# Performance work log

Measured on AMD Instinct MI355X. Metric: run time of the kernel, lower is better.

Reference implementation:

```python
import jax, jax.numpy as jnp
from jax import lax
import numpy as np

MAL = 10  # max_atom_len

def _conv1d(x, w, b):
    # x: [N,C,L], w: [O,I,K], 'same' padding for K=3 (pad 1)
    pad = (w.shape[-1] - 1) // 2
    y = lax.conv_general_dilated(x, w, (1,), [(pad, pad)], dimension_numbers=('NCH', 'OIH', 'NCH'))
    return y + b[None, :, None]

def _maxpool2(x):
    return lax.reduce_window(x, -jnp.inf, lax.max, (1, 1, 2), (1, 1, 2), 'VALID')

def setup_inputs():
    key = jax.random.key(0)
    ks = jax.random.split(key, 32)
    def p(i, shape):
        return 0.05 * jax.random.normal(ks[i], shape, jnp.float32)
    bs, seq, C, L = 128, 128, 6, 20
    D, H = 64, 256
    return {
        'x': jax.random.normal(ks[0], (bs, seq, C, L), jnp.float32),
        'imu_mask': jnp.ones((bs, seq, C, L), jnp.float32),
        'imu_len': jax.random.randint(ks[1], (bs,), 1, seq + 1),
        'c1_w': p(2, (16, 6, 3)), 'c1_b': p(3, (16,)),
        'c2_w': p(4, (32, 16, 3)), 'c2_b': p(5, (32,)),
        'c3_w': p(6, (32, 32, 3)), 'c3_b': p(7, (32,)),
        'br_w': p(8, (64, D)), 'br_b': p(9, (D,)),
        'f1_w': p(10, (D, H)), 'f1_b': p(11, (H,)),
        'f2_w': p(12, (H, D)), 'f2_b': p(13, (D,)),
        'd1_w': p(14, (16, 32, 5)), 'd1_b': p(15, (32,)),
        'd2_w': p(16, (6, 32, 3)), 'd2_b': p(17, (6,)),
        'ae1_w': p(18, (32, D, 3)), 'ae1_b': p(19, (32,)),
        'ae2_w': p(20, (16, 32, 3)), 'ae2_b': p(21, (16,)),
        'ae3_w': p(22, (80, 32)), 'ae3_b': p(23, (32,)),
        'ad1_w': p(24, (32, H)), 'ad1_b': p(25, (H,)),
        'ad2_w': p(26, (H, 6 * MAL * seq)), 'ad2_b': p(27, (6 * MAL * seq,)),
    }

def reference(x, imu_mask, c1_w, c1_b, c2_w, c2_b, c3_w, c3_b, br_w, br_b,
              f1_w, f1_b, f2_w, f2_b, d1_w, d1_b, d2_w, d2_b,
              ae1_w, ae1_b, ae2_w, ae2_b, ae3_w, ae3_b,
              ad1_w, ad1_b, ad2_w, ad2_b, imu_len):
    bs, seq, C, L = x.shape
    N = bs * seq
    # --- CNN encoder: [N,6,20] -> [N,32,2] -> flat 64 ---
    h = _maxpool2(jax.nn.relu(_conv1d(x.reshape(N, C, L), c1_w, c1_b)))  # [N,16,10]
    h = _maxpool2(jax.nn.relu(_conv1d(h, c2_w, c2_b)))                   # [N,32,5]
    h = _maxpool2(jax.nn.relu(_conv1d(h, c3_w, c3_b)))                   # [N,32,2]
    cnn_out = h.reshape(N, -1)
    bridge_out = jax.nn.sigmoid(cnn_out @ br_w + br_b)  # [N,D]
    D = bridge_out.shape[1]
    # --- forecast branch ---
    forcast_in3 = bridge_out.reshape(bs, seq, D)
    shft = jnp.pad(forcast_in3, ((0, 0), (1, 0), (0, 0)))[:, :-1]  # shift right by 1
    fmask = jnp.ones((bs, seq, D), jnp.float32).at[:, 0, :].set(0.0).reshape(N, D)
    fmask = fmask * imu_mask[:, :, 0, 0].reshape(N, 1)
    forcast_in = forcast_in3.reshape(N, D)
    feat = jax.nn.relu(shft.reshape(N, D) @ f1_w + f1_b)
    forcast = feat @ f2_w + f2_b
    forcast_loss = jnp.mean(jnp.square((forcast - forcast_in) * fmask), axis=1)  # [N]
    loss2d = forcast_loss.reshape(bs, seq)
    # --- host-side segmentation (mirrors original sort/argwhere/.item() loop) ---
    scores = np.asarray(forcast_loss * fmask[:, 0])
    k = int(scores.shape[0] * 0.2)
    cutoff = float(np.sort(scores)[::-1][:k].min())
    l2 = np.asarray(loss2d)
    seg_lists = []
    for b in range(bs):
        idxs = np.nonzero(l2[b] > cutoff)[0]
        segs = []
        if idxs.shape[0] > 0:
            for i in range(idxs.shape[0] - 1):
                if int(idxs[i + 1] - idxs[i]) > MAL:
                    cur = int(idxs[i]); segs.append(cur)
                    while cur < int(idxs[i + 1]):
                        cur += MAL
                        if cur >= int(idxs[i + 1]):
                            break
                        segs.append(cur)
                else:
                    segs.append(int(idxs[i]))
            segs.append(int(idxs[-1]))
        seg_lists.append(segs)
    # --- build variable-length atoms (left-pad / left-crop to fixed widths) ---
    bridge_np = np.asarray(forcast_in3)
    x_np = np.asarray(x)
    Wtot = MAL * seq
    feats, atoms, masks = [], [], []
    for b in range(bs):
        last = 0
        for e in seg_lists[b]:
            f = bridge_np[b, last:e]  # [n,D]
            pad = MAL - f.shape[0]
            fp = np.concatenate([np.zeros((pad, D), np.float32), f], 0) if pad >= 0 else f[-pad:]
            a = x_np[b, last:e].transpose(1, 0, 2).reshape(C, -1)  # [C, n*L]
            ap = Wtot - a.shape[1]
            if ap >= 0:
                apad = np.concatenate([np.zeros((C, ap), np.float32), a], 1)
                m = np.zeros((C, Wtot), np.float32); m[:, ap:] = 1.0
            else:
                apad = a[:, -ap:]; m = np.ones((C, Wtot), np.float32)
            feats.append(fp); atoms.append(apad); masks.append(m)
            last = e
    if len(feats) == 0:  # degenerate guard
        feats = [np.zeros((MAL, D), np.float32)]
        atoms = [np.zeros((C, Wtot), np.float32)]
        masks = [np.zeros((C, Wtot), np.float32)]
    A = len(feats)
    atom_features = jnp.asarray(np.stack(feats)).swapaxes(1, 2)  # [A,D,MAL]
    imu_atoms = jnp.asarray(np.stack(atoms))                      # [A,C,Wtot]
    imu_atoms_mask = jnp.asarray(np.stack(masks))
    # --- atom encoder / decoder ---
    ha = _maxpool2(jax.nn.relu(_conv1d(atom_features, ae1_w, ae1_b)))  # [A,32,5]
    ha = jax.nn.relu(_conv1d(ha, ae2_w, ae2_b))                        # [A,16,5]
    emb = ha.reshape(A, -1) @ ae3_w + ae3_b                            # [A,32]
    hd = jax.nn.relu(emb @ ad1_w + ad1_b)
    atom_gen = (hd @ ad2_w + ad2_b).reshape(A, C, Wtot)
    # --- imu decoder: [N,16,4] -> [N,6,20] ---
    bridge_resh = bridge_out.reshape(N, 16, 4)
    # non-overlapping transpose conv (kernel=stride=5): 4 -> 20
    g = jnp.einsum('nci,cok->noik', bridge_resh, d1_w).reshape(N, 32, 20)
    g = jax.nn.relu(g + d1_b[None, :, None])
    imu_gen = _conv1d(g, d2_w, d2_b).reshape(bs, seq, C, L)
    return (imu_gen, atom_gen, imu_atoms_mask, imu_atoms, bridge_resh,
            forcast_in, forcast, fmask, forcast_loss)
```

## Files before the change

### kernel.cpp

```cpp
#include <hip/hip_runtime.h>
#include <math.h>


#define NWIN 16384
#define SEQ  128
#define BS   128
#define KSEL 3276
#define SEGSTRIDE 160
#define RECCAP 18432

typedef __attribute__((ext_vector_type(8))) short short8v;
typedef __attribute__((ext_vector_type(4))) float float4v;

__device__ inline unsigned short bf16rne(float f) {
    unsigned u = __float_as_uint(f);
    unsigned r = u + 0x7FFFu + ((u >> 16) & 1u);
    return (unsigned short)(r >> 16);
}

__global__ __launch_bounds__(256) void k_encoder(
        const float* __restrict__ x,
        const float* __restrict__ c1w, const float* __restrict__ c1b,
        const float* __restrict__ c2w, const float* __restrict__ c2b,
        const float* __restrict__ c3w, const float* __restrict__ c3b,
        const float* __restrict__ brw, const float* __restrict__ brb,
        float* __restrict__ bridge, float* __restrict__ out_resh,
        float* __restrict__ out_fin) {
    __shared__ float c1wt[288];
    __shared__ float c2wt[1536];
    __shared__ float c3wt[3072];
    __shared__ float brws[4096];
    __shared__ float c1bs[16], c2bs[32], c3bs[32], brbs[64];
    __shared__ float xs[4][128], c1s[4][160], c2s[4][160], c3s[4][64];

    int tid = threadIdx.x;
    for (int i = tid; i < 288; i += 256) {
        int oc = i / 18, r = i - oc * 18, ic = r / 3, dk = r - ic * 3;
        c1wt[(ic * 3 + dk) * 16 + oc] = c1w[i];
    }
    for (int i = tid; i < 1536; i += 256) {
        int oc = i / 48, r = i - oc * 48, ic = r / 3, dk = r - ic * 3;
        c2wt[(ic * 3 + dk) * 32 + oc] = c2w[i];
    }
    for (int i = tid; i < 3072; i += 256) {
        int oc = i / 96, r = i - oc * 96, ic = r / 3, dk = r - ic * 3;
        c3wt[(ic * 3 + dk) * 32 + oc] = c3w[i];
    }
    for (int i = tid; i < 4096; i += 256) brws[i] = brw[i];
    if (tid < 16) c1bs[tid] = c1b[tid];
    else if (tid < 48) c2bs[tid - 16] = c2b[tid - 16];
    else if (tid < 80) c3bs[tid - 48] = c3b[tid - 48];
    else if (tid < 144) brbs[tid - 80] = brb[tid - 80];

    int wv = tid >> 6, lane = tid & 63;
    int n = blockIdx.x * 4 + wv;
    const float* xr = x + (size_t)n * 120;
    if (lane < 60) ((float2*)&xs[wv][0])[lane] = ((const float2*)xr)[lane];
    __syncthreads();

    {
        int oc = lane >> 2, tg = lane & 3;
        float bb = c1bs[oc];
        float acc[3][2];
#pragma unroll
        for (int j = 0; j < 3; ++j) { acc[j][0] = bb; acc[j][1] = bb; }
        for (int ic = 0; ic < 6; ++ic) {
            float w0 = c1wt[(ic * 3 + 0) * 16 + oc];
            float w1 = c1wt[(ic * 3 + 1) * 16 + oc];
            float w2 = c1wt[(ic * 3 + 2) * 16 + oc];
            const float* ar = &xs[wv][ic * 20];
#pragma unroll
            for (int j = 0; j < 3; ++j) {
                int t = tg + 4 * j;
                if (t < 10) {
#pragma unroll
                    for (int q = 0; q < 2; ++q) {
                        int p = 2 * t + q;
                        float a0 = (p >= 1) ? ar[p - 1] : 0.f;
                        float a1 = ar[p];
                        float a2 = (p + 1 < 20) ? ar[p + 1] : 0.f;
                        acc[j][q] += a0 * w0 + a1 * w1 + a2 * w2;
                    }
                }
            }
        }
#pragma unroll
        for (int j = 0; j < 3; ++j) {
            int t = tg + 4 * j;
            if (t < 10) c1s[wv][oc * 10 + t] = fmaxf(fmaxf(acc[j][0], acc[j][1]), 0.f);
        }
    }
    __syncthreads();

    {
        int oc = lane >> 1, tg = lane & 1;
        float bb = c2bs[oc];
        float acc[3][2];
#pragma unroll
        for (int j = 0; j < 3; ++j) { acc[j][0] = bb; acc[j][1] = bb; }
        for (int ic = 0; ic < 16; ++ic) {
            float w0 = c2wt[(ic * 3 + 0) * 32 + oc];
            float w1 = c2wt[(ic * 3 + 1) * 32 + oc];
            float w2 = c2wt[(ic * 3 + 2) * 32 + oc];
            const float* ar = &c1s[wv][ic * 10];
#pragma unroll
            for (int j = 0; j < 3; ++j) {
                int t = tg + 2 * j;
                if (t < 5) {
#pragma unroll
                    for (int q = 0; q < 2; ++q) {
                        int p = 2 * t + q;
                        float a0 = (p >= 1) ? ar[p - 1] : 0.f;
                        float a1 = ar[p];
                        float a2 = (p + 1 < 10) ? ar[p + 1] : 0.f;
                        acc[j][q] += a0 * w0 + a1 * w1 + a2 * w2;
                    }
                }
            }
        }
#pragma unroll
        for (int j = 0; j < 3; ++j) {
            int t = tg + 2 * j;
            if (t < 5) c2s[wv][oc * 5 + t] = fmaxf(fmaxf(acc[j][0], acc[j][1]), 0.f);
        }
    }
    __syncthreads();

    {
        int oc = lane >> 1, tp = lane & 1;
        float bb = c3bs[oc];
        float acc0 = bb, acc1 = bb;
        for (int ic = 0; ic < 32; ++ic) {
            float w0 = c3wt[(ic * 3 + 0) * 32 + oc];
            float w1 = c3wt[(ic * 3 + 1) * 32 + oc];
            float w2 = c3wt[(ic * 3 + 2) * 32 + oc];
            const float* ar = &c2s[wv][ic * 5];
            {
                int p = 2 * tp;
                float a0 = (p >= 1) ? ar[p - 1] : 0.f;
                acc0 += a0 * w0 + ar[p] * w1 + ar[p + 1] * w2;
            }
            {
                int p = 2 * tp + 1;
                acc1 += ar[p - 1] * w0 + ar[p] * w1 + ((p + 1 < 5) ? ar[p + 1] : 0.f) * w2;
            }
        }
        c3s[wv][lane] = fmaxf(fmaxf(acc0, acc1), 0.f);
    }
    __syncthreads();

    {
        float acc = brbs[lane];
        for (int i = 0; i < 64; ++i) acc += c3s[wv][i] * brws[i * 64 + lane];
        float v = 1.f / (1.f + expf(-acc));
        size_t o = (size_t)n * 64 + lane;
        bridge[o] = v; out_resh[o] = v; out_fin[o] = v;
    }
}

__global__ void k_f1(const float* __restrict__ bridge, const float* __restrict__ w,
                     const float* __restrict__ b, float* __restrict__ feat) {
    int n = blockIdx.x, h = threadIdx.x;
    int s = n & (SEQ - 1);
    float acc = b[h];
    if (s > 0) {
        const float* br = bridge + (n - 1) * 64;
        for (int d = 0; d < 64; ++d) acc += br[d] * w[d * 256 + h];
    }
    feat[n * 256 + h] = fmaxf(acc, 0.f);
}

__global__ void k_f2_loss(const float* __restrict__ feat, const float* __restrict__ bridge,
                          const float* __restrict__ w, const float* __restrict__ b,
                          const float* __restrict__ imu_mask,
                          float* __restrict__ out_fc, float* __restrict__ out_fmask,
                          float* __restrict__ out_loss, float* __restrict__ scores) {
    int n = blockIdx.x, d = threadIdx.x;
    const float* fr = feat + n * 256;
    float acc = b[d];
    for (int h = 0; h < 256; ++h) acc += fr[h] * w[h * 64 + d];
    out_fc[n * 64 + d] = acc;
    int s = n & (SEQ - 1);
    float mval = (s == 0) ? 0.f : imu_mask[(size_t)n * 120];
    out_fmask[n * 64 + d] = mval;
    float diff = (acc - bridge[n * 64 + d]) * mval;
    float sq = diff * diff;
#pragma unroll
    for (int off = 32; off; off >>= 1) sq += __shfl_down(sq, off);
    if (d == 0) {
        float loss = sq * (1.f / 64.f);
        out_loss[n] = loss;
        scores[n] = loss * mval;
    }
}

__global__ void k_select(const float* __restrict__ scores, float* __restrict__ cutoff) {
    __shared__ unsigned hist[256];
    __shared__ unsigned sh_prefix;
    __shared__ int sh_k;
    int tid = threadIdx.x;
    if (tid == 0) { sh_prefix = 0u; sh_k = KSEL; }
    __syncthreads();
    for (int shift = 24; shift >= 0; shift -= 8) {
        hist[tid] = 0u;
        __syncthreads();
        unsigned prefix = sh_prefix;
        unsigned pmask = (shift == 24) ? 0u : (0xFFFFFFFFu << (shift + 8));
        for (int i = tid; i < NWIN; i += 256) {
            unsigned u = __float_as_uint(scores[i]);
            if ((u & pmask) == prefix) atomicAdd(&hist[(u >> shift) & 255u], 1u);
        }
        __syncthreads();
        if (tid == 0) {
            int kk = sh_k;
            for (int bin = 255; bin >= 0; --bin) {
                int c = (int)hist[bin];
                if (kk <= c) { sh_prefix = prefix | ((unsigned)bin << shift); sh_k = kk; break; }
                kk -= c;
            }
        }
        __syncthreads();
    }
    if (tid == 0) *cutoff = __uint_as_float(sh_prefix);
}

__global__ void k_segments(const float* __restrict__ loss, const float* __restrict__ cutoff_p,
                           int* __restrict__ segs, int* __restrict__ counts) {
    int b = threadIdx.x;
    if (b >= BS) return;
    float cutoff = *cutoff_p;
    int* my = segs + b * SEGSTRIDE;
    int cnt = 0, prev = 0;
    bool has = false;
    for (int s = 0; s < SEQ; ++s) {
        if (loss[b * SEQ + s] > cutoff) {
            if (has) {
                if (s - prev > 10) {
                    my[cnt++] = prev;
                    int cur = prev;
                    while (cur < s) {
                        cur += 10;
                        if (cur >= s) break;
                        my[cnt++] = cur;
                    }
                } else {
                    my[cnt++] = prev;
                }
            }
            has = true; prev = s;
        }
    }
    if (has) my[cnt++] = prev;
    counts[b] = cnt;
}

__global__ void k_emit(const int* __restrict__ counts, const int* __restrict__ segs,
                       int* __restrict__ rec_b, int* __restrict__ rec_last,
                       int* __restrict__ rec_e, int* __restrict__ total_out) {
    __shared__ int offs[BS + 1];
    int tid = threadIdx.x;
    if (tid == 0) {
        int acc = 0;
        for (int b = 0; b < BS; ++b) { offs[b] = acc; acc += counts[b]; }
        offs[BS] = acc;
        *total_out = acc;
        if (acc == 0) { rec_b[0] = 0; rec_last[0] = 0; rec_e[0] = 0; }
    }
    __syncthreads();
    int b = tid;
    int o = offs[b], c = counts[b];
    for (int j = 0; j < c; ++j) {
        int idx = o + j;
        if (idx >= RECCAP) break;
        rec_b[idx] = b;
        rec_last[idx] = (j > 0) ? segs[b * SEGSTRIDE + j - 1] : 0;
        rec_e[idx] = segs[b * SEGSTRIDE + j];
    }
}

__global__ void k_gather_atoms(const int* __restrict__ rec_b, const int* __restrict__ rec_last,
                               const int* __restrict__ rec_e, const float* __restrict__ x,
                               float* __restrict__ out_atoms, float* __restrict__ out_mask, int A) {
    int gid = blockIdx.x * blockDim.x + threadIdx.x;
    if (gid >= A * 7680) return;
    int a = gid / 7680, rem = gid % 7680, c = rem / 1280, wcol = rem % 1280;
    int b = rec_b[a], last = rec_last[a], e = rec_e[a];
    int W = (e - last) * 20;
    int sc = wcol - (1280 - W);
    float v = 0.f, m = 0.f;
    if (sc >= 0 && sc < W) {
        int t = sc / 20, l = sc % 20;
        v = x[((b * SEQ + last + t) * 6 + c) * 20 + l];
        m = 1.f;
    }
    out_atoms[gid] = v;
    out_mask[gid] = m;
}

__global__ __launch_bounds__(256) void k_ae2(
        const int* __restrict__ rec_b, const int* __restrict__ rec_last,
        const int* __restrict__ rec_e, const float* __restrict__ bridge,
        const float* __restrict__ ae1w, const float* __restrict__ ae1b,
        const float* __restrict__ ae2w, const float* __restrict__ ae2b,
        const float* __restrict__ ae3w, const float* __restrict__ ae3b,
        const float* __restrict__ ad1w, const float* __restrict__ ad1b,
        unsigned short* __restrict__ hd, int A) {
    __shared__ float ae1wt[6144];
    __shared__ float ae2wt[1536];
    __shared__ float ae3ws[2560];
    __shared__ float ae1bs[32], ae2bs[16], ae3bs[32];
    __shared__ float af_s[8][640];
    __shared__ float c1p[8][160];
    __shared__ float h2s[8][80];
    __shared__ float embs[32][8];

    int tid = threadIdx.x;
    int a0 = blockIdx.x * 8;

    for (int i = tid; i < 6144; i += 256) {
        int o = i / 192, r = i - o * 192, ic = r / 3, dk = r - ic * 3;
        ae1wt[(ic * 3 + dk) * 32 + o] = ae1w[i];
    }
    for (int i = tid; i < 1536; i += 256) {
        int c = i / 96, r = i - c * 96, ic = r / 3, dk = r - ic * 3;
        ae2wt[(ic * 3 + dk) * 16 + c] = ae2w[i];
    }
    for (int i = tid; i < 2560; i += 256) ae3ws[i] = ae3w[i];
    if (tid < 32) ae1bs[tid] = ae1b[tid];
    else if (tid < 48) ae2bs[tid - 32] = ae2b[tid - 32];
    else if (tid < 80) ae3bs[tid - 48] = ae3b[tid - 48];

    int wv = tid >> 6, lane = tid & 63;
#pragma unroll
    for (int sg = 0; sg < 2; ++sg) {
        int seg = wv * 2 + sg;
        int ac = a0 + seg; if (ac > A - 1) ac = A - 1;
        int b = rec_b[ac], last = rec_last[ac], e = rec_e[ac];
#pragma unroll
        for (int r = 0; r < 10; ++r) {
            int src = e - 10 + r;
            float v = (src >= last) ? bridge[(size_t)(b * SEQ + src) * 64 + lane] : 0.f;
            af_s[seg][lane * 10 + r] = v;
        }
    }
    __syncthreads();

    {
        int seg = wv * 2 + (lane >> 5);
        int o = lane & 31;
        const float* afl = af_s[seg];
        float bb = ae1bs[o];
        float acc[10];
#pragma unroll
        for (int p = 0; p < 10; ++p) acc[p] = bb;
        for (int ic = 0; ic < 64; ++ic) {
            float av[10];
#pragma unroll
            for (int r = 0; r < 10; ++r) av[r] = afl[ic * 10 + r];
            float w0 = ae1wt[(ic * 3 + 0) * 32 + o];
            float w1 = ae1wt[(ic * 3 + 1) * 32 + o];
            float w2 = ae1wt[(ic * 3 + 2) * 32 + o];
            acc[0] += av[0] * w1 + av[1] * w2;
#pragma unroll
            for (int p = 1; p < 9; ++p)
                acc[p] += av[p - 1] * w0 + av[p] * w1 + av[p + 1] * w2;
            acc[9] += av[8] * w0 + av[9] * w1;
        }
#pragma unroll
        for (int t = 0; t < 5; ++t)
            c1p[seg][o * 5 + t] = fmaxf(fmaxf(acc[2 * t], acc[2 * t + 1]), 0.f);
    }
    __syncthreads();

    {
        int seg = wv * 2 + (lane >> 5);
        int c = (lane & 31) >> 1, th = lane & 1;
        const float* cp = c1p[seg];
        float bb = ae2bs[c];
        float acc2[3] = {bb, bb, bb};
        for (int ic = 0; ic < 32; ++ic) {
            float m[5];
#pragma unroll
            for (int t = 0; t < 5; ++t) m[t] = cp[ic * 5 + t];
            float w0 = ae2wt[(ic * 3 + 0) * 16 + c];
            float w1 = ae2wt[(ic * 3 + 1) * 16 + c];
            float w2 = ae2wt[(ic * 3 + 2) * 16 + c];
#pragma unroll
            for (int j = 0; j < 3; ++j) {
                int t = th + 2 * j;
                if (t < 5) {
                    float am1 = (t > 0) ? m[t - 1] : 0.f;
                    float ap1 = (t < 4) ? m[t + 1] : 0.f;
                    acc2[j] += am1 * w0 + m[t] * w1 + ap1 * w2;
                }
            }
        }
#pragma unroll
        for (int j = 0; j < 3; ++j) {
            int t = th + 2 * j;
            if (t < 5) h2s[seg][c * 5 + t] = fmaxf(acc2[j], 0.f);
        }
    }
    __syncthreads();

    {
        int seg = wv * 2 + (lane >> 5);
        int o = lane & 31;
        float acc = ae3bs[o];
        const float* hh = h2s[seg];
        for (int i = 0; i < 80; ++i) acc += hh[i] * ae3ws[i * 32 + o];
        embs[o][seg] = acc;
    }
    __syncthreads();

    {
        int idx = tid;
        float bb = ad1b[idx];
        float acc[8];
#pragma unroll
        for (int s = 0; s < 8; ++s) acc[s] = bb;
        for (int o = 0; o < 32; ++o) {
            float wq = ad1w[o * 256 + idx];
#pragma unroll
            for (int s = 0; s < 8; ++s) acc[s] += embs[o][s] * wq;
        }
#pragma unroll
        for (int s = 0; s < 8; ++s) {
            int a = a0 + s;
            if (a < A) hd[(size_t)a * 256 + idx] = bf16rne(fmaxf(acc[s], 0.f));
        }
    }
}

__global__ __launch_bounds__(256) void k_wtrans(const float* __restrict__ w,
                                                unsigned short* __restrict__ wbT) {
    __shared__ float tile[64][65];
    int n0 = blockIdx.x * 64, k0 = blockIdx.y * 64;
    int tid = threadIdx.x;
    int c = tid & 63;
    for (int r = tid >> 6; r < 64; r += 4)
        tile[r][c] = w[(size_t)(k0 + r) * 7680 + n0 + c];
    __syncthreads();
    int n = tid >> 4, kq = (tid & 15) * 4;
    for (int nn = n; nn < 64; nn += 16) {
        unsigned p0 = (unsigned)bf16rne(tile[kq + 0][nn]) |
                      ((unsigned)bf16rne(tile[kq + 1][nn]) << 16);
        unsigned p1 = (unsigned)bf16rne(tile[kq + 2][nn]) |
                      ((unsigned)bf16rne(tile[kq + 3][nn]) << 16);
        unsigned* dst = (unsigned*)&wbT[(size_t)(n0 + nn) * 256 + k0 + kq];
        dst[0] = p0; dst[1] = p1;
    }
}

#define LSTR 264
__global__ __launch_bounds__(256) void k_ad2m(const unsigned short* __restrict__ hdb,
                                              const unsigned short* __restrict__ wbT,
                                              const float* __restrict__ bias,
                                              float* __restrict__ out, int A) {
    __shared__ unsigned short wt[64 * LSTR];
    int tid = threadIdx.x;
    int m0 = blockIdx.x * 64;
    int n0 = blockIdx.y * 64;

    {
        const short8v* src = (const short8v*)(wbT + (size_t)n0 * 256);
#pragma unroll
        for (int i = 0; i < 8; ++i) {
            int flat = tid + 256 * i;
            int row = flat >> 5, ch = flat & 31;
            short8v v = src[flat];
            *(short8v*)&wt[row * LSTR + ch * 8] = v;
        }
    }
    __syncthreads();

    int wv = tid >> 6, lane = tid & 63;
    int rc = lane & 15;
    int koff = (lane >> 4) * 8;
    float4v acc[4];
#pragma unroll
    for (int i = 0; i < 4; ++i) acc[i] = (float4v){0.f, 0.f, 0.f, 0.f};

    const short* ha = (const short*)hdb + (size_t)(m0 + wv * 16 + rc) * 256 + koff;
#pragma unroll
    for (int s = 0; s < 8; ++s) {
        short8v a = *(const short8v*)(ha + s * 32);
#pragma unroll
        for (int nt = 0; nt < 4; ++nt) {
            short8v b = *(const short8v*)((const short*)&wt[(nt * 16 + rc) * LSTR + s * 32 + koff]);
            acc[nt] = __builtin_amdgcn_mfma_f32_16x16x32_bf16(a, b, acc[nt], 0, 0, 0);
        }
    }

    int quad = lane >> 4;
#pragma unroll
    for (int nt = 0; nt < 4; ++nt) {
        int n = n0 + nt * 16 + rc;
        float bb = bias[n];
#pragma unroll
        for (int r = 0; r < 4; ++r) {
            int m = m0 + wv * 16 + quad * 4 + r;
            if (m < A) out[(size_t)m * 7680 + n] = acc[nt][r] + bb;
        }
    }
}

__global__ __launch_bounds__(256) void k_decoder(const float* __restrict__ bridge,
                          const float* __restrict__ d1w, const float* __restrict__ d1b,
                          const float* __restrict__ d2w, const float* __restrict__ d2b,
                          float* __restrict__ out) {
    __shared__ float d1wt[16 * 5 * 33];
    __shared__ float d2wt[576];
    __shared__ float d1bs[32], d2bs[8];
    __shared__ float brs[4][64];
    __shared__ float gs[4][640];
    int tid = threadIdx.x;
    for (int i = tid; i < 2560; i += 256) {
        int c = i / 160, r = i - c * 160, o = r / 5, kk = r - o * 5;
        d1wt[(c * 5 + kk) * 33 + o] = d1w[i];
    }
    for (int i = tid; i < 576; i += 256) {
        int oc = i / 96, r = i - oc * 96, ic = r / 3, dk = r - ic * 3;
        d2wt[(ic * 3 + dk) * 6 + oc] = d2w[i];
    }
    if (tid < 32) d1bs[tid] = d1b[tid];
    else if (tid < 38) d2bs[tid - 32] = d2b[tid - 32];
    int wv = tid >> 6, lane = tid & 63;
    int n = blockIdx.x * 4 + wv;
    brs[wv][lane] = bridge[(size_t)n * 64 + lane];
    __syncthreads();
    for (int idx = lane; idx < 640; idx += 64) {
        int o = idx / 20, p = idx - o * 20, i = p / 5, kk = p - i * 5;
        float acc = d1bs[o];
#pragma unroll
        for (int c = 0; c < 16; ++c) acc += brs[wv][c * 4 + i] * d1wt[(c * 5 + kk) * 33 + o];
        gs[wv][idx] = fmaxf(acc, 0.f);
    }
    __syncthreads();
    for (int idx = lane; idx < 120; idx += 64) {
        int oc = idx / 20, t = idx - oc * 20;
        float acc = d2bs[oc];
        for (int ic = 0; ic < 32; ++ic) {
            const float* gr = &gs[wv][ic * 20];
            float a0 = (t >= 1) ? gr[t - 1] : 0.f;
            float a1 = gr[t];
            float a2 = (t + 1 < 20) ? gr[t + 1] : 0.f;
            acc += a0 * d2wt[(ic * 3 + 0) * 6 + oc]
                 + a1 * d2wt[(ic * 3 + 1) * 6 + oc]
                 + a2 * d2wt[(ic * 3 + 2) * 6 + oc];
        }
        out[(size_t)n * 120 + idx] = acc;
    }
}

extern "C" void kernel_launch(void* const* d_in, const int* in_sizes, int n_in,
                              void* d_out, int out_size, void* d_ws, size_t ws_size,
                              hipStream_t stream) {
    const float* x        = (const float*)d_in[0];
    const float* imu_mask = (const float*)d_in[1];
    const float* c1_w = (const float*)d_in[3];
    const float* c1_b = (const float*)d_in[4];
    const float* c2_w = (const float*)d_in[5];
    const float* c2_b = (const float*)d_in[6];
    const float* c3_w = (const float*)d_in[7];
    const float* c3_b = (const float*)d_in[8];
    const float* br_w = (const float*)d_in[9];
    const float* br_b = (const float*)d_in[10];
    const float* f1_w = (const float*)d_in[11];
    const float* f1_b = (const float*)d_in[12];
    const float* f2_w = (const float*)d_in[13];
    const float* f2_b = (const float*)d_in[14];
    const float* d1_w = (const float*)d_in[15];
    const float* d1_b = (const float*)d_in[16];
    const float* d2_w = (const float*)d_in[17];
    const float* d2_b = (const float*)d_in[18];
    const float* ae1_w = (const float*)d_in[19];
    const float* ae1_b = (const float*)d_in[20];
    const float* ae2_w = (const float*)d_in[21];
    const float* ae2_b = (const float*)d_in[22];
    const float* ae3_w = (const float*)d_in[23];
    const float* ae3_b = (const float*)d_in[24];
    const float* ad1_w = (const float*)d_in[25];
    const float* ad1_b = (const float*)d_in[26];
    const float* ad2_w = (const float*)d_in[27];
    const float* ad2_b = (const float*)d_in[28];

    int A = (out_size - 6176768) / 23040;
    if (A < 1) A = 1;

    float* out = (float*)d_out;
    size_t o_imu_gen  = 0;
    size_t o_atom_gen = 1966080;
    size_t o_mask     = o_atom_gen + (size_t)A * 7680;
    size_t o_atoms    = o_mask + (size_t)A * 7680;
    size_t o_resh     = o_atoms + (size_t)A * 7680;
    size_t o_fin      = o_resh + 1048576;
    size_t o_fc       = o_fin + 1048576;
    size_t o_fmask    = o_fc + 1048576;
    size_t o_loss     = o_fmask + 1048576;

    float* wsf = (float*)d_ws;
    int*   wsi = (int*)d_ws;
    const size_t W_BRIDGE = 0;
    const size_t W_FEAT   = W_BRIDGE + 1048576;
    const size_t W_SCORES = W_FEAT + 4194304;
    const size_t W_CUTOFF = W_SCORES + 16384;
    const size_t MW       = W_CUTOFF + 64;
    int* counts   = wsi + MW;
    int* total    = wsi + MW + 128;
    int* segs     = wsi + MW + 192;
    int* rec_b    = wsi + MW + 192 + BS * SEGSTRIDE;
    int* rec_last = rec_b + RECCAP;
    int* rec_e    = rec_last + RECCAP;
    size_t HD_OFF = MW + 192 + BS * SEGSTRIDE + 3 * RECCAP;
    unsigned short* hd  = (unsigned short*)(wsf + HD_OFF);
    unsigned short* wbT = (unsigned short*)(wsf + HD_OFF + (size_t)RECCAP * 128);

    hipMemsetAsync(rec_b, 0, 3 * RECCAP * sizeof(int), stream);

    const int T = 256;
    dim3 gt(120, 4);
    k_wtrans<<<gt, 256, 0, stream>>>(ad2_w, wbT);
    k_encoder<<<NWIN / 4, 256, 0, stream>>>(x, c1_w, c1_b, c2_w, c2_b, c3_w, c3_b,
                                            br_w, br_b, wsf + W_BRIDGE,
                                            out + o_resh, out + o_fin);
    k_f1<<<NWIN, 256, 0, stream>>>(wsf + W_BRIDGE, f1_w, f1_b, wsf + W_FEAT);
    k_f2_loss<<<NWIN, 64, 0, stream>>>(wsf + W_FEAT, wsf + W_BRIDGE, f2_w, f2_b, imu_mask,
                                       out + o_fc, out + o_fmask, out + o_loss, wsf + W_SCORES);
    k_select<<<1, 256, 0, stream>>>(wsf + W_SCORES, wsf + W_CUTOFF);
    k_segments<<<1, 128, 0, stream>>>(out + o_loss, wsf + W_CUTOFF, segs, counts);
    k_emit<<<1, 128, 0, stream>>>(counts, segs, rec_b, rec_last, rec_e, total);
    k_gather_atoms<<<(A * 7680 + T - 1) / T, T, 0, stream>>>(rec_b, rec_last, rec_e, x,
                                                             out + o_atoms, out + o_mask, A);
    k_ae2<<<(A + 7) / 8, 256, 0, stream>>>(rec_b, rec_last, rec_e, wsf + W_BRIDGE,
                                           ae1_w, ae1_b, ae2_w, ae2_b, ae3_w, ae3_b,
                                           ad1_w, ad1_b, hd, A);
    dim3 g2((A + 63) / 64, 120);
    k_ad2m<<<g2, 256, 0, stream>>>(hd, wbT, ad2_b, out + o_atom_gen, A);
    k_decoder<<<NWIN / 4, 256, 0, stream>>>(wsf + W_BRIDGE, d1_w, d1_b, d2_w, d2_b,
                                            out + o_imu_gen);
}
```

Measured before the change: 901.1 us.

## Fuse forecast MLP layers and merge selection/segment/emit kernels

Replaces the separate f1 and f2+loss kernels with one k_forecast kernel. It stages both 64x256 weight matrices in LDS, keeps the hidden features in shared memory instead of a global scratch buffer, and has each wave process 8 windows. It also merges the radix top-k select, segment building and record emission into a single single-block kernel with per-wave histograms and LDS segment storage, which removes launches and global round trips. The trade-off is about 130KB of LDS per forecast block, which limits occupancy to one block per CU, and only 256 blocks in total.

```diff
diff --git a/kernel.cpp b/kernel.cpp
--- a/kernel.cpp
+++ b/kernel.cpp
@@ -158,107 +158,132 @@
     }
 }
 
-__global__ void k_f1(const float* __restrict__ bridge, const float* __restrict__ w,
-                     const float* __restrict__ b, float* __restrict__ feat) {
-    int n = blockIdx.x, h = threadIdx.x;
-    int s = n & (SEQ - 1);
-    float acc = b[h];
-    if (s > 0) {
-        const float* br = bridge + (n - 1) * 64;
-        for (int d = 0; d < 64; ++d) acc += br[d] * w[d * 256 + h];
-    }
-    feat[n * 256 + h] = fmaxf(acc, 0.f);
-}
-
-__global__ void k_f2_loss(const float* __restrict__ feat, const float* __restrict__ bridge,
-                          const float* __restrict__ w, const float* __restrict__ b,
-                          const float* __restrict__ imu_mask,
-                          float* __restrict__ out_fc, float* __restrict__ out_fmask,
-                          float* __restrict__ out_loss, float* __restrict__ scores) {
-    int n = blockIdx.x, d = threadIdx.x;
-    const float* fr = feat + n * 256;
-    float acc = b[d];
-    for (int h = 0; h < 256; ++h) acc += fr[h] * w[h * 64 + d];
-    out_fc[n * 64 + d] = acc;
-    int s = n & (SEQ - 1);
-    float mval = (s == 0) ? 0.f : imu_mask[(size_t)n * 120];
-    out_fmask[n * 64 + d] = mval;
-    float diff = (acc - bridge[n * 64 + d]) * mval;
-    float sq = diff * diff;
-#pragma unroll
-    for (int off = 32; off; off >>= 1) sq += __shfl_down(sq, off);
-    if (d == 0) {
-        float loss = sq * (1.f / 64.f);
-        out_loss[n] = loss;
-        scores[n] = loss * mval;
-    }
-}
-
-__global__ void k_select(const float* __restrict__ scores, float* __restrict__ cutoff) {
-    __shared__ unsigned hist[256];
+__global__ __launch_bounds__(512) void k_forecast(
+        const float* __restrict__ bridge,
+        const float* __restrict__ w1, const float* __restrict__ b1,
+        const float* __restrict__ w2, const float* __restrict__ b2,
+        const float* __restrict__ imu_mask,
+        float* __restrict__ out_fc, float* __restrict__ out_fmask,
+        float* __restrict__ out_loss, float* __restrict__ scores) {
+    __shared__ float w1s[16384];
+    __shared__ float w2s[16384];
+    __shared__ float b1s[256], b2s[64];
+    __shared__ float fts[8][256];
+
+    int tid = threadIdx.x;
+    {
+        const float4* s1 = (const float4*)w1;
+        const float4* s2 = (const float4*)w2;
+        float4* d1 = (float4*)w1s;
+        float4* d2 = (float4*)w2s;
+        for (int i = tid; i < 4096; i += 512) { d1[i] = s1[i]; d2[i] = s2[i]; }
+    }
+    if (tid < 256) b1s[tid] = b1[tid];
+    else if (tid < 320) b2s[tid - 256] = b2[tid - 256];
+    __syncthreads();
+
+    int wv = tid >> 6, lane = tid & 63;
+    int nbase = blockIdx.x * 64 + wv * 8;
+#pragma unroll 1
+    for (int i = 0; i < 8; ++i) {
+        int n = nbase + i;
+        int s = n & (SEQ - 1);
+        float acc[4];
+#pragma unroll
+        for (int j = 0; j < 4; ++j) acc[j] = b1s[lane + 64 * j];
+        if (s > 0) {
+            float brv = bridge[(size_t)(n - 1) * 64 + lane];
+#pragma unroll 4
+            for (int d = 0; d < 64; ++d) {
+                float bd = __shfl(brv, d);
+#pragma unroll
+                for (int j = 0; j < 4; ++j)
+                    acc[j] += bd * w1s[d * 256 + lane + 64 * j];
+            }
+        }
+#pragma unroll
+        for (int j = 0; j < 4; ++j) fts[wv][lane + 64 * j] = fmaxf(acc[j], 0.f);
+        float fa = b2s[lane];
+#pragma unroll 8
+        for (int h = 0; h < 256; ++h) fa += fts[wv][h] * w2s[h * 64 + lane];
+        out_fc[(size_t)n * 64 + lane] = fa;
+        float mval = (s == 0) ? 0.f : imu_mask[(size_t)n * 120];
+        out_fmask[(size_t)n * 64 + lane] = mval;
+        float diff = (fa - bridge[(size_t)n * 64 + lane]) * mval;
+        float sq = diff * diff;
+#pragma unroll
+        for (int off = 32; off; off >>= 1) sq += __shfl_down(sq, off);
+        if (lane == 0) {
+            float loss = sq * (1.f / 64.f);
+            out_loss[n] = loss;
+            scores[n] = loss * mval;
+        }
+    }
+}
+
+__global__ __launch_bounds__(256) void k_postsel(
+        const float* __restrict__ scores, const float* __restrict__ loss,
+        int* __restrict__ rec_b, int* __restrict__ rec_last,
+        int* __restrict__ rec_e, int* __restrict__ total_out) {
+    __shared__ unsigned hist[4][256];
     __shared__ unsigned sh_prefix;
     __shared__ int sh_k;
-    int tid = threadIdx.x;
+    __shared__ int segs[BS][SEGSTRIDE];
+    __shared__ int counts[BS];
+    __shared__ int offs[BS + 1];
+    int tid = threadIdx.x, wv = tid >> 6;
     if (tid == 0) { sh_prefix = 0u; sh_k = KSEL; }
     __syncthreads();
     for (int shift = 24; shift >= 0; shift -= 8) {
-        hist[tid] = 0u;
+#pragma unroll
+        for (int w = 0; w < 4; ++w) hist[w][tid] = 0u;
         __syncthreads();
         unsigned prefix = sh_prefix;
         unsigned pmask = (shift == 24) ? 0u : (0xFFFFFFFFu << (shift + 8));
         for (int i = tid; i < NWIN; i += 256) {
             unsigned u = __float_as_uint(scores[i]);
-            if ((u & pmask) == prefix) atomicAdd(&hist[(u >> shift) & 255u], 1u);
+            if ((u & pmask) == prefix) atomicAdd(&hist[wv][(u >> shift) & 255u], 1u);
         }
         __syncthreads();
         if (tid == 0) {
             int kk = sh_k;
             for (int bin = 255; bin >= 0; --bin) {
-                int c = (int)hist[bin];
+                int c = (int)(hist[0][bin] + hist[1][bin] + hist[2][bin] + hist[3][bin]);
                 if (kk <= c) { sh_prefix = prefix | ((unsigned)bin << shift); sh_k = kk; break; }
                 kk -= c;
             }
         }
         __syncthreads();
     }
-    if (tid == 0) *cutoff = __uint_as_float(sh_prefix);
-}
-
-__global__ void k_segments(const float* __restrict__ loss, const float* __restrict__ cutoff_p,
-                           int* __restrict__ segs, int* __restrict__ counts) {
-    int b = threadIdx.x;
-    if (b >= BS) return;
-    float cutoff = *cutoff_p;
-    int* my = segs + b * SEGSTRIDE;
-    int cnt = 0, prev = 0;
-    bool has = false;
-    for (int s = 0; s < SEQ; ++s) {
-        if (loss[b * SEQ + s] > cutoff) {
-            if (has) {
-                if (s - prev > 10) {
-                    my[cnt++] = prev;
-                    int cur = prev;
-                    while (cur < s) {
-                        cur += 10;
-                        if (cur >= s) break;
-                        my[cnt++] = cur;
+    float cutoff = __uint_as_float(sh_prefix);
+
+    if (tid < BS) {
+        int b = tid;
+        int* my = segs[b];
+        int cnt = 0, prev = 0;
+        bool has = false;
+        for (int s = 0; s < SEQ; ++s) {
+            if (loss[b * SEQ + s] > cutoff) {
+                if (has) {
+                    if (s - prev > 10) {
+                        my[cnt++] = prev;
+                        int cur = prev;
+                        while (cur < s) {
+                            cur += 10;
+                            if (cur >= s) break;
+                            my[cnt++] = cur;
+                        }
+                    } else {
+                        my[cnt++] = prev;
                     }
-                } else {
-                    my[cnt++] = prev;
                 }
-            }
-            has = true; prev = s;
-        }
-    }
-    if (has) my[cnt++] = prev;
-    counts[b] = cnt;
-}
-
-__global__ void k_emit(const int* __restrict__ counts, const int* __restrict__ segs,
-                       int* __restrict__ rec_b, int* __restrict__ rec_last,
-                       int* __restrict__ rec_e, int* __restrict__ total_out) {
-    __shared__ int offs[BS + 1];
-    int tid = threadIdx.x;
+                has = true; prev = s;
+            }
+        }
+        if (has) my[cnt++] = prev;
+        counts[b] = cnt;
+    }
+    __syncthreads();
     if (tid == 0) {
         int acc = 0;
         for (int b = 0; b < BS; ++b) { offs[b] = acc; acc += counts[b]; }
@@ -267,14 +292,16 @@
         if (acc == 0) { rec_b[0] = 0; rec_last[0] = 0; rec_e[0] = 0; }
     }
     __syncthreads();
-    int b = tid;
-    int o = offs[b], c = counts[b];
-    for (int j = 0; j < c; ++j) {
-        int idx = o + j;
-        if (idx >= RECCAP) break;
-        rec_b[idx] = b;
-        rec_last[idx] = (j > 0) ? segs[b * SEGSTRIDE + j - 1] : 0;
-        rec_e[idx] = segs[b * SEGSTRIDE + j];
+    if (tid < BS) {
+        int b = tid;
+        int o = offs[b], c = counts[b];
+        for (int j = 0; j < c; ++j) {
+            int idx = o + j;
+            if (idx >= RECCAP) break;
+            rec_b[idx] = b;
+            rec_last[idx] = (j > 0) ? segs[b][j - 1] : 0;
+            rec_e[idx] = segs[b][j];
+        }
     }
 }
 
@@ -615,6 +642,7 @@
     size_t HD_OFF = MW + 192 + BS * SEGSTRIDE + 3 * RECCAP;
     unsigned short* hd  = (unsigned short*)(wsf + HD_OFF);
     unsigned short* wbT = (unsigned short*)(wsf + HD_OFF + (size_t)RECCAP * 128);
+    (void)counts; (void)segs;
 
     hipMemsetAsync(rec_b, 0, 3 * RECCAP * sizeof(int), stream);
 
@@ -624,12 +652,11 @@
     k_encoder<<<NWIN / 4, 256, 0, stream>>>(x, c1_w, c1_b, c2_w, c2_b, c3_w, c3_b,
                                             br_w, br_b, wsf + W_BRIDGE,
                                             out + o_resh, out + o_fin);
-    k_f1<<<NWIN, 256, 0, stream>>>(wsf + W_BRIDGE, f1_w, f1_b, wsf + W_FEAT);
-    k_f2_loss<<<NWIN, 64, 0, stream>>>(wsf + W_FEAT, wsf + W_BRIDGE, f2_w, f2_b, imu_mask,
-                                       out + o_fc, out + o_fmask, out + o_loss, wsf + W_SCORES);
-    k_select<<<1, 256, 0, stream>>>(wsf + W_SCORES, wsf + W_CUTOFF);
-    k_segments<<<1, 128, 0, stream>>>(out + o_loss, wsf + W_CUTOFF, segs, counts);
-    k_emit<<<1, 128, 0, stream>>>(counts, segs, rec_b, rec_last, rec_e, total);
+    k_forecast<<<NWIN / 64, 512, 0, stream>>>(wsf + W_BRIDGE, f1_w, f1_b, f2_w, f2_b,
+                                              imu_mask, out + o_fc, out + o_fmask,
+                                              out + o_loss, wsf + W_SCORES);
+    k_postsel<<<1, 256, 0, stream>>>(wsf + W_SCORES, out + o_loss,
+                                     rec_b, rec_last, rec_e, total);
     k_gather_atoms<<<(A * 7680 + T - 1) / T, T, 0, stream>>>(rec_b, rec_last, rec_e, x,
                                                              out + o_atoms, out + o_mask, A);
     k_ae2<<<(A + 7) / 8, 256, 0, stream>>>(rec_b, rec_last, rec_e, wsf + W_BRIDGE,
```

After: 893.1 us. Within noise of the previous version (-0.9%).
